# Kernel optimization log

Measured on AMD Instinct MI355X. Metric: run time of the kernel, lower is better.

Reference implementation:

```python
import jax, jax.numpy as jnp
import numpy as np

N = 50000      # nodes
E = 500000     # edges
D = 128        # in_dim == out_dim
L = 4          # encoder_layers
G = 64         # graphs in batch
FIXED = 10000  # fixed_input_dim
BN_EPS = 1e-5


def setup_inputs() -> dict:
    key = jax.random.key(0)
    ks = jax.random.split(key, 14)
    s = 0.05
    feat_id = jax.random.randint(ks[0], (N,), 0, FIXED)
    edge_index = jax.random.randint(ks[1], (2, E), 0, N)
    # sorted graph assignment guaranteeing all G graphs are non-empty
    batch = (jnp.arange(N) * G) // N
    return {
        "feat_id": feat_id,
        "edge_index": edge_index,
        "batch": batch,
        # value_projection: Linear(FIXED, D); store weight.T as a lookup table
        "value_proj_w": jax.random.normal(ks[2], (FIXED, D)) * s,
        "value_proj_b": jax.random.normal(ks[3], (D,)) * s,
        "deg_emb": jax.random.normal(ks[4], (1001, D)) * s,
        # stacked per-layer GIN MLP params: Linear -> BN -> ReLU -> Linear
        "mlp_w1": jax.random.normal(ks[5], (L, D, D)) * s,
        "mlp_b1": jax.random.normal(ks[6], (L, D)) * s,
        "bn1_g": 1.0 + 0.1 * jax.random.normal(ks[7], (L, D)),
        "bn1_b": 0.1 * jax.random.normal(ks[8], (L, D)),
        "mlp_w2": jax.random.normal(ks[9], (L, D, D)) * s,
        "mlp_b2": jax.random.normal(ks[10], (L, D)) * s,
        # outer per-layer BatchNorm1d
        "bn2_g": 1.0 + 0.1 * jax.random.normal(ks[11], (L, D)),
        "bn2_b": 0.1 * jax.random.normal(ks[12], (L, D)),
    }


def _bn(x, g, b):
    # BatchNorm1d in training mode: batch stats over the node axis, biased var
    mu = jnp.mean(x, axis=0)
    var = jnp.mean(jnp.square(x - mu), axis=0)
    return g * (x - mu) * jax.lax.rsqrt(var + BN_EPS) + b


def reference(feat_id, edge_index, batch, value_proj_w, value_proj_b, deg_emb,
              mlp_w1, mlp_b1, bn1_g, bn1_b, mlp_w2, mlp_b2, bn2_g, bn2_b):
    src, dst = edge_index[0], edge_index[1]
    # one_hot(feat_id % FIXED) @ W.T + b  ==  gather of transposed weight rows
    h_attr = value_proj_w[feat_id % FIXED] + value_proj_b  # [N, D]
    # in-degree embedding (clamped to [0, 1000])
    in_deg = jax.ops.segment_sum(jnp.ones((E,), jnp.int32), dst, num_segments=N)
    h = h_attr + deg_emb[jnp.clip(in_deg, 0, 1000)]
    for i in range(L):
        # GIN: sum_{j in N(v)} h_j + (1 + eps) * h_v, eps = 0 (learn_eps=False)
        agg = jax.ops.segment_sum(h[src], dst, num_segments=N) + h
        z = jax.nn.relu(_bn(agg @ mlp_w1[i] + mlp_b1[i], bn1_g[i], bn1_b[i]))
        z = z @ mlp_w2[i] + mlp_b2[i]
        h = jax.nn.relu(_bn(z, bn2_g[i], bn2_b[i]))
    # global mean pool per graph
    gsum = jax.ops.segment_sum(h, batch, num_segments=G)       # [G, D]
    cnt = jax.ops.segment_sum(jnp.ones((N, 1)), batch, num_segments=G)
    graph_feature = gsum / jnp.maximum(cnt, 1.0)
    return graph_feature, h
```

## Files before the change

kernel.cpp:

```cpp
#include <hip/hip_runtime.h>

#define NN 50000
#define NE 500000
#define DD 128
#define NL 4
#define NG 64
#define FIXED_DIM 10000
#define BN_EPS 1e-5f
#define NB 196

typedef unsigned short u16;
typedef unsigned int u32;
typedef __attribute__((ext_vector_type(8))) short bf16x8;
typedef __attribute__((ext_vector_type(4))) float f32x4;

__device__ __forceinline__ float bf2f(u16 u) {
    return __uint_as_float(((u32)u) << 16);
}
__device__ __forceinline__ u16 f2bf(float f) {
    u32 u = __float_as_uint(f);
    return (u16)((u + 0x7FFFu + ((u >> 16) & 1u)) >> 16);
}
__device__ __forceinline__ float ldf(const void* p, size_t i, int isbf) {
    return isbf ? bf2f(((const u16*)p)[i]) : ((const float*)p)[i];
}

__global__ void k_pre(const void* __restrict__ vb, int* __restrict__ flag,
                      const int* __restrict__ batch, int* __restrict__ goff,
                      float* __restrict__ zbase, int zwords) {
    int b = blockIdx.x, t = threadIdx.x;
    if (b == 0) {
        __shared__ int ok[256];
        float v = (t < 128) ? bf2f(((const u16*)vb)[t]) : 0.f;
        ok[t] = (t < 128) ? ((fabsf(v) < 1000.f) ? 1 : 0) : 1;
        __syncthreads();
        for (int off = 128; off; off >>= 1) {
            if (t < off) ok[t] &= ok[t + off];
            __syncthreads();
        }
        if (t == 0) *flag = ok[0];
    } else if (b == 1) {
        if (t <= NG) {
            int lo = 0, hi = NN;
            while (lo < hi) {
                int mid = (lo + hi) >> 1;
                if (batch[mid] < t) lo = mid + 1; else hi = mid;
            }
            goff[t] = lo;
        }
    } else {
        int i = (b - 2) * 256 + t;
        if (i < zwords) zbase[i] = 0.f;
    }
}

__global__ void k_cvt6(const void* b1, const void* b2, const void* g1,
                       const void* be1, const void* g2, const void* be2,
                       float* __restrict__ pc, const int* __restrict__ flag) {
    int t = blockIdx.x * 256 + threadIdx.x;
    if (t >= 6 * NL * DD) return;
    int p = t >> 9, j = t & 511;
    const void* s = (p == 0) ? b1 : (p == 1) ? b2 : (p == 2) ? g1
                  : (p == 3) ? be1 : (p == 4) ? g2 : be2;
    pc[t] = ldf(s, j, *flag);
}
__global__ void k_deg(const int* __restrict__ dst, int* __restrict__ deg) {
    int i = blockIdx.x * 256 + threadIdx.x;
    if (i < NE) atomicAdd(&deg[dst[i]], 1);
}

__global__ void k_scan1(const int* __restrict__ deg, int* __restrict__ bsum) {
    __shared__ int S[256];
    int b = blockIdx.x, t = threadIdx.x;
    int i = b * 256 + t;
    S[t] = (i < NN) ? deg[i] : 0;
    __syncthreads();
    for (int off = 128; off; off >>= 1) {
        if (t < off) S[t] += S[t + off];
        __syncthreads();
    }
    if (t == 0) bsum[b] = S[0];
}
__global__ void k_scan2(int* __restrict__ bsum) {
    __shared__ int S[256];
    int t = threadIdx.x;
    int v = (t < NB) ? bsum[t] : 0;
    S[t] = v;
    __syncthreads();
    for (int off = 1; off < 256; off <<= 1) {
        int x = (t >= off) ? S[t - off] : 0;
        __syncthreads();
        S[t] += x;
        __syncthreads();
    }
    if (t < NB) bsum[t] = S[t] - v;
}
__global__ void k_scan3(const int* __restrict__ deg, const int* __restrict__ bsum,
                        int* __restrict__ rowptr) {
    __shared__ int S[256];
    int b = blockIdx.x, t = threadIdx.x;
    int i = b * 256 + t;
    int v = (i < NN) ? deg[i] : 0;
    S[t] = v;
    __syncthreads();
    for (int off = 1; off < 256; off <<= 1) {
        int x = (t >= off) ? S[t - off] : 0;
        __syncthreads();
        S[t] += x;
        __syncthreads();
    }
    if (i < NN) rowptr[i] = bsum[b] + S[t] - v;
    if (i == NN - 1) rowptr[NN] = bsum[b] + S[t];
}

__global__ void k_fill(const int* __restrict__ src, const int* __restrict__ dst,
                       const int* __restrict__ rowptr, int* __restrict__ cursor,
                       int* __restrict__ colidx) {
    int e = blockIdx.x * 256 + threadIdx.x;
    if (e >= NE) return;
    int d = dst[e];
    int p = atomicAdd(&cursor[d], 1);
    colidx[rowptr[d] + p] = src[e];
}

__global__ void k_swz(const void* __restrict__ w1, const void* __restrict__ w2,
                      u16* __restrict__ Wsw, const int* __restrict__ flag) {
    int t = blockIdx.x * 256 + threadIdx.x;
    if (t >= 8 * 16384) return;
    int m    = t >> 14;
    int idx  = t & 16383;
    int nt   = idx >> 11;
    int ks   = (idx >> 9) & 3;
    int lane = (idx >> 3) & 63;
    int j    = idx & 7;
    int row = ks * 32 + (lane >> 4) * 8 + j;
    int col = nt * 16 + (lane & 15);
    const void* src = (m < 4) ? w1 : w2;
    size_t off = (size_t)(m & 3) * DD * DD + (size_t)row * DD + col;
    Wsw[t] = f2bf(ldf(src, off, *flag));
}

__global__ void k_init(const int* __restrict__ feat, const int* __restrict__ deg,
                       const void* __restrict__ vw, const void* __restrict__ vb,
                       const void* __restrict__ demb, u16* __restrict__ B,
                       const int* __restrict__ flag) {
    int t = blockIdx.x * 256 + threadIdx.x;
    if (t >= NN * DD) return;
    int n = t >> 7, c = t & 127;
    int isbf = *flag;
    int f = feat[n] % FIXED_DIM;
    int dg = min(deg[n], 1000);
    B[t] = f2bf(ldf(vw, (size_t)f * DD + c, isbf)
              + ldf(vb, c, isbf)
              + ldf(demb, (size_t)dg * DD + c, isbf));
}

template <bool AFF>
__global__ __launch_bounds__(256, 8) void k_aggr(
        const u16* __restrict__ B, const int* __restrict__ rowptr,
        const int* __restrict__ colidx,
        const float* __restrict__ gIn, const float* __restrict__ bIn,
        const float* __restrict__ sIn, const float* __restrict__ qIn,
        u16* __restrict__ Agg) {
    int n = blockIdx.x * 4 + (threadIdx.x >> 6);
    if (n >= NN) return;
    int c = (threadIdx.x & 63) * 2;
    float a0 = 1.f, b0 = 0.f, a1 = 1.f, b1 = 0.f;
    if (AFF) {
        float inv = 1.0f / (float)NN;
        float mu0 = sIn[c] * inv, mu1 = sIn[c + 1] * inv;
        float v0 = fmaxf(qIn[c] * inv - mu0 * mu0, 0.f);
        float v1 = fmaxf(qIn[c + 1] * inv - mu1 * mu1, 0.f);
        a0 = gIn[c] * rsqrtf(v0 + BN_EPS);
        a1 = gIn[c + 1] * rsqrtf(v1 + BN_EPS);
        b0 = bIn[c] - a0 * mu0;
        b1 = bIn[c + 1] - a1 * mu1;
    }
    u32 w = *(const u32*)&B[(size_t)n * DD + c];
    float x0 = bf2f((u16)(w & 0xFFFF)), x1 = bf2f((u16)(w >> 16));
    float s0 = AFF ? fmaxf(fmaf(a0, x0, b0), 0.f) : x0;
    float s1 = AFF ? fmaxf(fmaf(a1, x1, b1), 0.f) : x1;
    int lo = rowptr[n], hi = rowptr[n + 1];
    int j = lo;
    for (; j + 4 <= hi; j += 4) {
        int m0 = colidx[j], m1 = colidx[j + 1];
        int m2 = colidx[j + 2], m3 = colidx[j + 3];
        u32 w0 = *(const u32*)&B[(size_t)m0 * DD + c];
        u32 w1v = *(const u32*)&B[(size_t)m1 * DD + c];
        u32 w2v = *(const u32*)&B[(size_t)m2 * DD + c];
        u32 w3v = *(const u32*)&B[(size_t)m3 * DD + c];
        float y;
        y = bf2f((u16)(w0 & 0xFFFF)); s0 += AFF ? fmaxf(fmaf(a0, y, b0), 0.f) : y;
        y = bf2f((u16)(w0 >> 16));    s1 += AFF ? fmaxf(fmaf(a1, y, b1), 0.f) : y;
        y = bf2f((u16)(w1v & 0xFFFF)); s0 += AFF ? fmaxf(fmaf(a0, y, b0), 0.f) : y;
        y = bf2f((u16)(w1v >> 16));    s1 += AFF ? fmaxf(fmaf(a1, y, b1), 0.f) : y;
        y = bf2f((u16)(w2v & 0xFFFF)); s0 += AFF ? fmaxf(fmaf(a0, y, b0), 0.f) : y;
        y = bf2f((u16)(w2v >> 16));    s1 += AFF ? fmaxf(fmaf(a1, y, b1), 0.f) : y;
        y = bf2f((u16)(w3v & 0xFFFF)); s0 += AFF ? fmaxf(fmaf(a0, y, b0), 0.f) : y;
        y = bf2f((u16)(w3v >> 16));    s1 += AFF ? fmaxf(fmaf(a1, y, b1), 0.f) : y;
    }
    for (; j < hi; j++) {
        int m = colidx[j];
        w = *(const u32*)&B[(size_t)m * DD + c];
        x0 = bf2f((u16)(w & 0xFFFF)); x1 = bf2f((u16)(w >> 16));
        s0 += AFF ? fmaxf(fmaf(a0, x0, b0), 0.f) : x0;
        s1 += AFF ? fmaxf(fmaf(a1, x1, b1), 0.f) : x1;
    }
    *(u32*)&Agg[(size_t)n * DD + c] = ((u32)f2bf(s1) << 16) | (u32)f2bf(s0);
}

template <bool IN16, bool OUT16, bool AFF>
__global__ __launch_bounds__(256, 2) void k_gemm(
        const void* In, const u16* __restrict__ Wsw,
        const float* __restrict__ bias,
        const float* __restrict__ gIn, const float* __restrict__ bIn,
        const float* __restrict__ sIn, const float* __restrict__ qIn,
        void* Out, float* __restrict__ ssum, float* __restrict__ ssq,
        int nRows) {
    __shared__ u16 Wl[16384];
    __shared__ u16 At[128 * 136];
    __shared__ float affS[256];
    float* RedS = (float*)At;
    float* RedQ = RedS + 512;
    const int t = threadIdx.x;
    const int row0 = blockIdx.x * 128;

    if (AFF) {
        if (t < 128) {
            float inv = 1.0f / (float)NN;
            float mu = sIn[t] * inv;
            float var = fmaxf(qIn[t] * inv - mu * mu, 0.f);
            float a = gIn[t] * rsqrtf(var + BN_EPS);
            affS[t] = a;
            affS[128 + t] = bIn[t] - a * mu;
        }
        __syncthreads();
    }

    {
        const uint4* s = (const uint4*)Wsw;
        uint4* d = (uint4*)Wl;
        #pragma unroll
        for (int i = 0; i < 8; i++) d[t + i * 256] = s[t + i * 256];
    }
    if (IN16) {
        for (int i = t; i < 2048; i += 256) {
            int r  = i >> 4;
            int c8 = (i & 15) * 8;
            int gr = row0 + r;
            uint4 v = make_uint4(0u, 0u, 0u, 0u);
            if (gr < nRows) v = *(const uint4*)&((const u16*)In)[(size_t)gr * DD + c8];
            *(uint4*)&At[r * 136 + c8] = v;
        }
    } else {
        for (int i = t; i < 4096; i += 256) {
            int r  = i >> 5;
            int c4 = (i & 31) * 4;
            int gr = row0 + r;
            float4 v = make_float4(0.f, 0.f, 0.f, 0.f);
            if (gr < nRows) {
                v = *(const float4*)&((const float*)In)[(size_t)gr * DD + c4];
                if (AFF) {
                    v.x = fmaxf(fmaf(affS[c4 + 0], v.x, affS[128 + c4 + 0]), 0.f);
                    v.y = fmaxf(fmaf(affS[c4 + 1], v.y, affS[128 + c4 + 1]), 0.f);
                    v.z = fmaxf(fmaf(affS[c4 + 2], v.z, affS[128 + c4 + 2]), 0.f);
                    v.w = fmaxf(fmaf(affS[c4 + 3], v.w, affS[128 + c4 + 3]), 0.f);
                }
            }
            ushort4 o;
            o.x = f2bf(v.x); o.y = f2bf(v.y); o.z = f2bf(v.z); o.w = f2bf(v.w);
            *(ushort4*)&At[r * 136 + c4] = o;
        }
    }
    __syncthreads();

    const int w    = t >> 6;
    const int ln   = t & 63;
    const int quad = ln >> 4;
    const int lq   = ln & 15;

    f32x4 acc0[8], acc1[8];
    #pragma unroll
    for (int nt = 0; nt < 8; nt++) {
        acc0[nt] = (f32x4){0.f, 0.f, 0.f, 0.f};
        acc1[nt] = (f32x4){0.f, 0.f, 0.f, 0.f};
    }

    const u16* aRow0 = &At[(w * 32 + lq) * 136 + quad * 8];
    const u16* aRow1 = &At[(w * 32 + 16 + lq) * 136 + quad * 8];
    #pragma unroll
    for (int ks = 0; ks < 4; ks++) {
        bf16x8 a0 = *(const bf16x8*)&aRow0[ks * 32];
        bf16x8 a1 = *(const bf16x8*)&aRow1[ks * 32];
        #pragma unroll
        for (int nt = 0; nt < 8; nt++) {
            bf16x8 b = *(const bf16x8*)&Wl[((nt * 4 + ks) * 64 + ln) * 8];
            acc0[nt] = __builtin_amdgcn_mfma_f32_16x16x32_bf16(a0, b, acc0[nt], 0, 0, 0);
            acc1[nt] = __builtin_amdgcn_mfma_f32_16x16x32_bf16(a1, b, acc1[nt], 0, 0, 0);
        }
    }
    __syncthreads();

    const int rb0 = row0 + w * 32 + quad * 4;
    const int rb1 = rb0 + 16;
    #pragma unroll
    for (int nt = 0; nt < 8; nt++) {
        int col = nt * 16 + lq;
        float bv = bias[col];
        float s = 0.f, q = 0.f;
        #pragma unroll
        for (int r = 0; r < 4; r++) {
            int gr = rb0 + r;
            if (gr < nRows) {
                float val = acc0[nt][r] + bv;
                size_t o = (size_t)gr * DD + col;
                if (OUT16) ((u16*)Out)[o] = f2bf(val);
                else       ((float*)Out)[o] = val;
                s += val; q += val * val;
            }
        }
        #pragma unroll
        for (int r = 0; r < 4; r++) {
            int gr = rb1 + r;
            if (gr < nRows) {
                float val = acc1[nt][r] + bv;
                size_t o = (size_t)gr * DD + col;
                if (OUT16) ((u16*)Out)[o] = f2bf(val);
                else       ((float*)Out)[o] = val;
                s += val; q += val * val;
            }
        }
        s += __shfl_xor(s, 16); q += __shfl_xor(q, 16);
        s += __shfl_xor(s, 32); q += __shfl_xor(q, 32);
        if (quad == 0) { RedS[w * 128 + col] = s; RedQ[w * 128 + col] = q; }
    }
    __syncthreads();
    if (t < 128) {
        float s = RedS[t] + RedS[128 + t] + RedS[256 + t] + RedS[384 + t];
        float q = RedQ[t] + RedQ[128 + t] + RedQ[256 + t] + RedQ[384 + t];
        atomicAdd(&ssum[t], s);
        atomicAdd(&ssq[t], q);
    }
}

__global__ __launch_bounds__(256, 4) void k_update2(
        const u16* __restrict__ Bz,
        const float* __restrict__ gIn, const float* __restrict__ bIn,
        const float* __restrict__ sIn, const float* __restrict__ qIn,
        const int* __restrict__ batch, float* __restrict__ A,
        float* __restrict__ gsum) {
    const int t = threadIdx.x;
    const int c = t & 127;
    const int half = t >> 7;
    const int r0 = blockIdx.x * 64;
    float inv = 1.0f / (float)NN;
    float mu = sIn[c] * inv;
    float var = fmaxf(qIn[c] * inv - mu * mu, 0.f);
    float a = gIn[c] * rsqrtf(var + BN_EPS);
    float bb = bIn[c] - a * mu;
    float acc = 0.f;
    int curg = -1;
    for (int i = 0; i < 32; i++) {
        int r = r0 + half + 2 * i;
        if (r >= NN) break;
        int gg = batch[r];
        if (gg != curg) {
            if (curg >= 0) atomicAdd(&gsum[(size_t)curg * DD + c], acc);
            acc = 0.f; curg = gg;
        }
        float v = fmaxf(fmaf(a, bf2f(Bz[(size_t)r * DD + c]), bb), 0.f);
        A[(size_t)r * DD + c] = v;
        acc += v;
    }
    if (curg >= 0) atomicAdd(&gsum[(size_t)curg * DD + c], acc);
}

__global__ void k_pool2(const float* __restrict__ gsum, const int* __restrict__ goff,
                        float* __restrict__ out) {
    int t = blockIdx.x * 256 + threadIdx.x;
    int g = t >> 7;
    float cnt = fmaxf((float)(goff[g + 1] - goff[g]), 1.0f);
    out[t] = gsum[t] / cnt;
}

extern "C" void kernel_launch(void* const* d_in, const int* in_sizes, int n_in,
                              void* d_out, int out_size, void* d_ws, size_t ws_size,
                              hipStream_t stream) {
    const int* feat  = (const int*)d_in[0];
    const int* ei    = (const int*)d_in[1];
    const int* batch = (const int*)d_in[2];
    const void* vw   = d_in[3];
    const void* vb   = d_in[4];
    const void* demb = d_in[5];
    const void* w1   = d_in[6];
    const void* b1   = d_in[7];
    const void* g1   = d_in[8];
    const void* be1  = d_in[9];
    const void* w2   = d_in[10];
    const void* b2   = d_in[11];
    const void* g2   = d_in[12];
    const void* be2  = d_in[13];

    const int* src = ei;
    const int* dst = ei + NE;
    const size_t ND = (size_t)NN * DD;

    float* pc     = (float*)d_ws;
    int*   flag   = (int*)(pc + 3072);
    float* stats  = (float*)(flag + 64);
    float* gsum   = stats + 2048;
    int*   deg    = (int*)(gsum + 8192);
    int*   cursor = deg + NN;
    int*   bsum   = cursor + NN;
    int*   goff   = bsum + 256;
    int*   rowptr = goff + 128;
    int*   colidx = rowptr + NN + 64;
    u16*   Wsw    = (u16*)(colidx + NE);
    u16*   B      = Wsw + 8 * 16384;
    u16*   Agg16  = B + ND;

    float* b1c  = pc;
    float* b2c  = pc + 512;
    float* g1c  = pc + 1024;
    float* be1c = pc + 1536;
    float* g2c  = pc + 2048;
    float* be2c = pc + 2560;
    float* sum1 = stats;
    float* sq1  = stats + 512;
    float* sum2 = stats + 1024;
    float* sq2  = stats + 1536;

    float* outw = (float*)d_out;
    float* A    = outw + (size_t)NG * DD;

    const int zwords = 2048 + 8192 + NN + NN;
    const int gridND = (int)((ND + 255) / 256);
    const int gemmBlocks = (NN + 127) / 128;
    const int aggrBlocks = (NN + 3) / 4;

    k_pre<<<2 + (zwords + 255) / 256, 256, 0, stream>>>(vb, flag, batch, goff,
                                                        stats, zwords);
    k_cvt6<<<(6 * NL * DD + 255) / 256, 256, 0, stream>>>(b1, b2, g1, be1, g2, be2, pc, flag);
    k_swz<<<(8 * 16384) / 256, 256, 0, stream>>>(w1, w2, Wsw, flag);
    k_deg<<<(NE + 255) / 256, 256, 0, stream>>>(dst, deg);
    k_scan1<<<NB, 256, 0, stream>>>(deg, bsum);
    k_scan2<<<1, 256, 0, stream>>>(bsum);
    k_scan3<<<NB, 256, 0, stream>>>(deg, bsum, rowptr);
    k_fill<<<(NE + 255) / 256, 256, 0, stream>>>(src, dst, rowptr, cursor, colidx);
    k_init<<<gridND, 256, 0, stream>>>(feat, deg, vw, vb, demb, B, flag);

    for (int l = 0; l < NL; l++) {
        const u16* W1l = Wsw + (size_t)l * 16384;
        const u16* W2l = Wsw + (size_t)(4 + l) * 16384;
        if (l == 0) {
            k_aggr<false><<<aggrBlocks, 256, 0, stream>>>(
                B, rowptr, colidx, nullptr, nullptr, nullptr, nullptr, Agg16);
        } else {
            k_aggr<true><<<aggrBlocks, 256, 0, stream>>>(
                B, rowptr, colidx, g2c + (l - 1) * 128, be2c + (l - 1) * 128,
                sum2 + (l - 1) * 128, sq2 + (l - 1) * 128, Agg16);
        }
        k_gemm<true, false, false><<<gemmBlocks, 256, 0, stream>>>(
            Agg16, W1l, b1c + l * 128, nullptr, nullptr, nullptr, nullptr,
            A, sum1 + l * 128, sq1 + l * 128, NN);
        k_gemm<false, true, true><<<gemmBlocks, 256, 0, stream>>>(
            A, W2l, b2c + l * 128, g1c + l * 128, be1c + l * 128,
            sum1 + l * 128, sq1 + l * 128,
            B, sum2 + l * 128, sq2 + l * 128, NN);
    }
    k_update2<<<(NN + 63) / 64, 256, 0, stream>>>(
        B, g2c + 3 * 128, be2c + 3 * 128, sum2 + 3 * 128, sq2 + 3 * 128,
        batch, A, gsum);
    k_pool2<<<(NG * DD + 255) / 256, 256, 0, stream>>>(gsum, goff, outw);
}
```

Measured before the change: 527.7 us.

## Fuse neighbor aggregation into first GEMM and merge setup kernels

Neighbor aggregation is fused with the first MLP linear layer. Each 64-row block gathers neighbor sums into shared memory as bf16, then multiplies by the weight tile with MFMA and accumulates BN statistics, so the intermediate aggregate never round-trips through global memory. Several small setup kernels are merged: the param conversion with the weight swizzle, scan1 with scan2 via a last-block semaphore, scan3 with init, and the final update with pooling. This cuts launch count. In exchange the fused kernel uses much more LDS and has lower occupancy (launch bounds 3), which may hurt latency hiding for the irregular gathers.

```diff
diff --git a/kernel.cpp b/kernel.cpp
--- a/kernel.cpp
+++ b/kernel.cpp
@@ -54,23 +54,43 @@
     }
 }
 
-__global__ void k_cvt6(const void* b1, const void* b2, const void* g1,
-                       const void* be1, const void* g2, const void* be2,
-                       float* __restrict__ pc, const int* __restrict__ flag) {
-    int t = blockIdx.x * 256 + threadIdx.x;
-    if (t >= 6 * NL * DD) return;
-    int p = t >> 9, j = t & 511;
-    const void* s = (p == 0) ? b1 : (p == 1) ? b2 : (p == 2) ? g1
-                  : (p == 3) ? be1 : (p == 4) ? g2 : be2;
-    pc[t] = ldf(s, j, *flag);
-}
+__global__ void k_cvtswz(const void* b1, const void* b2, const void* g1,
+                         const void* be1, const void* g2, const void* be2,
+                         const void* __restrict__ w1, const void* __restrict__ w2,
+                         float* __restrict__ pc, u16* __restrict__ Wsw,
+                         const int* __restrict__ flag) {
+    int b = blockIdx.x, tt = threadIdx.x;
+    if (b < 12) {
+        int t = b * 256 + tt;
+        int p = t >> 9, j = t & 511;
+        const void* s = (p == 0) ? b1 : (p == 1) ? b2 : (p == 2) ? g1
+                      : (p == 3) ? be1 : (p == 4) ? g2 : be2;
+        pc[t] = ldf(s, j, *flag);
+    } else {
+        int t = (b - 12) * 256 + tt;
+        int m    = t >> 14;
+        int idx  = t & 16383;
+        int nt   = idx >> 11;
+        int ks   = (idx >> 9) & 3;
+        int lane = (idx >> 3) & 63;
+        int j    = idx & 7;
+        int row = ks * 32 + (lane >> 4) * 8 + j;
+        int col = nt * 16 + (lane & 15);
+        const void* src = (m < 4) ? w1 : w2;
+        size_t off = (size_t)(m & 3) * DD * DD + (size_t)row * DD + col;
+        Wsw[t] = f2bf(ldf(src, off, *flag));
+    }
+}
+
 __global__ void k_deg(const int* __restrict__ dst, int* __restrict__ deg) {
     int i = blockIdx.x * 256 + threadIdx.x;
     if (i < NE) atomicAdd(&deg[dst[i]], 1);
 }
 
-__global__ void k_scan1(const int* __restrict__ deg, int* __restrict__ bsum) {
+__global__ void k_scan12(const int* __restrict__ deg, int* __restrict__ bsum,
+                         int* __restrict__ sem) {
     __shared__ int S[256];
+    __shared__ int lastB;
     int b = blockIdx.x, t = threadIdx.x;
     int i = b * 256 + t;
     S[t] = (i < NN) ? deg[i] : 0;
@@ -79,12 +99,15 @@
         if (t < off) S[t] += S[t + off];
         __syncthreads();
     }
-    if (t == 0) bsum[b] = S[0];
-}
-__global__ void k_scan2(int* __restrict__ bsum) {
-    __shared__ int S[256];
-    int t = threadIdx.x;
-    int v = (t < NB) ? bsum[t] : 0;
+    if (t == 0) {
+        atomicExch(&bsum[b], S[0]);
+        __threadfence();
+        lastB = (atomicAdd(&sem[0], 1) == gridDim.x - 1);
+    }
+    __syncthreads();
+    if (!lastB) return;
+    __threadfence();
+    int v = (t < NB) ? atomicAdd(&bsum[t], 0) : 0;
     S[t] = v;
     __syncthreads();
     for (int off = 1; off < 256; off <<= 1) {
@@ -95,22 +118,38 @@
     }
     if (t < NB) bsum[t] = S[t] - v;
 }
-__global__ void k_scan3(const int* __restrict__ deg, const int* __restrict__ bsum,
-                        int* __restrict__ rowptr) {
+
+__global__ void k_scan3init(const int* __restrict__ deg, const int* __restrict__ bsum,
+                            int* __restrict__ rowptr,
+                            const int* __restrict__ feat, const void* __restrict__ vw,
+                            const void* __restrict__ vb, const void* __restrict__ demb,
+                            u16* __restrict__ B, const int* __restrict__ flag) {
     __shared__ int S[256];
     int b = blockIdx.x, t = threadIdx.x;
-    int i = b * 256 + t;
-    int v = (i < NN) ? deg[i] : 0;
-    S[t] = v;
-    __syncthreads();
-    for (int off = 1; off < 256; off <<= 1) {
-        int x = (t >= off) ? S[t - off] : 0;
+    if (b < NB) {
+        int i = b * 256 + t;
+        int v = (i < NN) ? deg[i] : 0;
+        S[t] = v;
         __syncthreads();
-        S[t] += x;
-        __syncthreads();
-    }
-    if (i < NN) rowptr[i] = bsum[b] + S[t] - v;
-    if (i == NN - 1) rowptr[NN] = bsum[b] + S[t];
+        for (int off = 1; off < 256; off <<= 1) {
+            int x = (t >= off) ? S[t - off] : 0;
+            __syncthreads();
+            S[t] += x;
+            __syncthreads();
+        }
+        if (i < NN) rowptr[i] = bsum[b] + S[t] - v;
+        if (i == NN - 1) rowptr[NN] = bsum[b] + S[t];
+    } else {
+        int idx = (b - NB) * 256 + t;
+        if (idx >= NN * DD) return;
+        int n = idx >> 7, c = idx & 127;
+        int isbf = *flag;
+        int f = feat[n] % FIXED_DIM;
+        int dg = min(deg[n], 1000);
+        B[idx] = f2bf(ldf(vw, (size_t)f * DD + c, isbf)
+                    + ldf(vb, c, isbf)
+                    + ldf(demb, (size_t)dg * DD + c, isbf));
+    }
 }
 
 __global__ void k_fill(const int* __restrict__ src, const int* __restrict__ dst,
@@ -123,90 +162,129 @@
     colidx[rowptr[d] + p] = src[e];
 }
 
-__global__ void k_swz(const void* __restrict__ w1, const void* __restrict__ w2,
-                      u16* __restrict__ Wsw, const int* __restrict__ flag) {
-    int t = blockIdx.x * 256 + threadIdx.x;
-    if (t >= 8 * 16384) return;
-    int m    = t >> 14;
-    int idx  = t & 16383;
-    int nt   = idx >> 11;
-    int ks   = (idx >> 9) & 3;
-    int lane = (idx >> 3) & 63;
-    int j    = idx & 7;
-    int row = ks * 32 + (lane >> 4) * 8 + j;
-    int col = nt * 16 + (lane & 15);
-    const void* src = (m < 4) ? w1 : w2;
-    size_t off = (size_t)(m & 3) * DD * DD + (size_t)row * DD + col;
-    Wsw[t] = f2bf(ldf(src, off, *flag));
-}
-
-__global__ void k_init(const int* __restrict__ feat, const int* __restrict__ deg,
-                       const void* __restrict__ vw, const void* __restrict__ vb,
-                       const void* __restrict__ demb, u16* __restrict__ B,
-                       const int* __restrict__ flag) {
-    int t = blockIdx.x * 256 + threadIdx.x;
-    if (t >= NN * DD) return;
-    int n = t >> 7, c = t & 127;
-    int isbf = *flag;
-    int f = feat[n] % FIXED_DIM;
-    int dg = min(deg[n], 1000);
-    B[t] = f2bf(ldf(vw, (size_t)f * DD + c, isbf)
-              + ldf(vb, c, isbf)
-              + ldf(demb, (size_t)dg * DD + c, isbf));
-}
-
 template <bool AFF>
-__global__ __launch_bounds__(256, 8) void k_aggr(
-        const u16* __restrict__ B, const int* __restrict__ rowptr,
-        const int* __restrict__ colidx,
+__global__ __launch_bounds__(256, 3) void k_ag1(
+        const u16* __restrict__ Bv, const int* __restrict__ rowptr,
+        const int* __restrict__ colidx, const u16* __restrict__ Wsw,
+        const float* __restrict__ bias,
         const float* __restrict__ gIn, const float* __restrict__ bIn,
         const float* __restrict__ sIn, const float* __restrict__ qIn,
-        u16* __restrict__ Agg) {
-    int n = blockIdx.x * 4 + (threadIdx.x >> 6);
-    if (n >= NN) return;
-    int c = (threadIdx.x & 63) * 2;
-    float a0 = 1.f, b0 = 0.f, a1 = 1.f, b1 = 0.f;
-    if (AFF) {
-        float inv = 1.0f / (float)NN;
-        float mu0 = sIn[c] * inv, mu1 = sIn[c + 1] * inv;
-        float v0 = fmaxf(qIn[c] * inv - mu0 * mu0, 0.f);
-        float v1 = fmaxf(qIn[c + 1] * inv - mu1 * mu1, 0.f);
-        a0 = gIn[c] * rsqrtf(v0 + BN_EPS);
-        a1 = gIn[c + 1] * rsqrtf(v1 + BN_EPS);
-        b0 = bIn[c] - a0 * mu0;
-        b1 = bIn[c + 1] - a1 * mu1;
-    }
-    u32 w = *(const u32*)&B[(size_t)n * DD + c];
-    float x0 = bf2f((u16)(w & 0xFFFF)), x1 = bf2f((u16)(w >> 16));
-    float s0 = AFF ? fmaxf(fmaf(a0, x0, b0), 0.f) : x0;
-    float s1 = AFF ? fmaxf(fmaf(a1, x1, b1), 0.f) : x1;
-    int lo = rowptr[n], hi = rowptr[n + 1];
-    int j = lo;
-    for (; j + 4 <= hi; j += 4) {
-        int m0 = colidx[j], m1 = colidx[j + 1];
-        int m2 = colidx[j + 2], m3 = colidx[j + 3];
-        u32 w0 = *(const u32*)&B[(size_t)m0 * DD + c];
-        u32 w1v = *(const u32*)&B[(size_t)m1 * DD + c];
-        u32 w2v = *(const u32*)&B[(size_t)m2 * DD + c];
-        u32 w3v = *(const u32*)&B[(size_t)m3 * DD + c];
-        float y;
-        y = bf2f((u16)(w0 & 0xFFFF)); s0 += AFF ? fmaxf(fmaf(a0, y, b0), 0.f) : y;
-        y = bf2f((u16)(w0 >> 16));    s1 += AFF ? fmaxf(fmaf(a1, y, b1), 0.f) : y;
-        y = bf2f((u16)(w1v & 0xFFFF)); s0 += AFF ? fmaxf(fmaf(a0, y, b0), 0.f) : y;
-        y = bf2f((u16)(w1v >> 16));    s1 += AFF ? fmaxf(fmaf(a1, y, b1), 0.f) : y;
-        y = bf2f((u16)(w2v & 0xFFFF)); s0 += AFF ? fmaxf(fmaf(a0, y, b0), 0.f) : y;
-        y = bf2f((u16)(w2v >> 16));    s1 += AFF ? fmaxf(fmaf(a1, y, b1), 0.f) : y;
-        y = bf2f((u16)(w3v & 0xFFFF)); s0 += AFF ? fmaxf(fmaf(a0, y, b0), 0.f) : y;
-        y = bf2f((u16)(w3v >> 16));    s1 += AFF ? fmaxf(fmaf(a1, y, b1), 0.f) : y;
-    }
-    for (; j < hi; j++) {
-        int m = colidx[j];
-        w = *(const u32*)&B[(size_t)m * DD + c];
-        x0 = bf2f((u16)(w & 0xFFFF)); x1 = bf2f((u16)(w >> 16));
-        s0 += AFF ? fmaxf(fmaf(a0, x0, b0), 0.f) : x0;
-        s1 += AFF ? fmaxf(fmaf(a1, x1, b1), 0.f) : x1;
-    }
-    *(u32*)&Agg[(size_t)n * DD + c] = ((u32)f2bf(s1) << 16) | (u32)f2bf(s0);
+        float* __restrict__ Out, float* __restrict__ ssum, float* __restrict__ ssq) {
+    __shared__ u16 Wl[16384];
+    __shared__ u16 At[64 * 136];
+    float* RedS = (float*)At;
+    float* RedQ = RedS + 512;
+    const int t = threadIdx.x;
+    const int w = t >> 6;
+    const int ln = t & 63;
+    const int row0 = blockIdx.x * 64;
+
+    {
+        const uint4* s = (const uint4*)Wsw;
+        uint4* d = (uint4*)Wl;
+        #pragma unroll
+        for (int i = 0; i < 8; i++) d[t + i * 256] = s[t + i * 256];
+    }
+
+    {
+        const int c = ln * 2;
+        float a0 = 1.f, b0 = 0.f, a1 = 1.f, b1 = 0.f;
+        if (AFF) {
+            float inv = 1.0f / (float)NN;
+            float mu0 = sIn[c] * inv, mu1 = sIn[c + 1] * inv;
+            float v0 = fmaxf(qIn[c] * inv - mu0 * mu0, 0.f);
+            float v1 = fmaxf(qIn[c + 1] * inv - mu1 * mu1, 0.f);
+            a0 = gIn[c] * rsqrtf(v0 + BN_EPS);
+            a1 = gIn[c + 1] * rsqrtf(v1 + BN_EPS);
+            b0 = bIn[c] - a0 * mu0;
+            b1 = bIn[c + 1] - a1 * mu1;
+        }
+        for (int rr = 0; rr < 16; rr++) {
+            int lr = w * 16 + rr;
+            int gr = row0 + lr;
+            float s0 = 0.f, s1 = 0.f;
+            if (gr < NN) {
+                u32 wd = *(const u32*)&Bv[(size_t)gr * DD + c];
+                float x0 = bf2f((u16)(wd & 0xFFFF)), x1 = bf2f((u16)(wd >> 16));
+                s0 = AFF ? fmaxf(fmaf(a0, x0, b0), 0.f) : x0;
+                s1 = AFF ? fmaxf(fmaf(a1, x1, b1), 0.f) : x1;
+                int lo = rowptr[gr], hi = rowptr[gr + 1];
+                int j = lo;
+                for (; j + 4 <= hi; j += 4) {
+                    int m0 = colidx[j], m1 = colidx[j + 1];
+                    int m2 = colidx[j + 2], m3 = colidx[j + 3];
+                    u32 wd0 = *(const u32*)&Bv[(size_t)m0 * DD + c];
+                    u32 wd1 = *(const u32*)&Bv[(size_t)m1 * DD + c];
+                    u32 wd2 = *(const u32*)&Bv[(size_t)m2 * DD + c];
+                    u32 wd3 = *(const u32*)&Bv[(size_t)m3 * DD + c];
+                    float y;
+                    y = bf2f((u16)(wd0 & 0xFFFF)); s0 += AFF ? fmaxf(fmaf(a0, y, b0), 0.f) : y;
+                    y = bf2f((u16)(wd0 >> 16));    s1 += AFF ? fmaxf(fmaf(a1, y, b1), 0.f) : y;
+                    y = bf2f((u16)(wd1 & 0xFFFF)); s0 += AFF ? fmaxf(fmaf(a0, y, b0), 0.f) : y;
+                    y = bf2f((u16)(wd1 >> 16));    s1 += AFF ? fmaxf(fmaf(a1, y, b1), 0.f) : y;
+                    y = bf2f((u16)(wd2 & 0xFFFF)); s0 += AFF ? fmaxf(fmaf(a0, y, b0), 0.f) : y;
+                    y = bf2f((u16)(wd2 >> 16));    s1 += AFF ? fmaxf(fmaf(a1, y, b1), 0.f) : y;
+                    y = bf2f((u16)(wd3 & 0xFFFF)); s0 += AFF ? fmaxf(fmaf(a0, y, b0), 0.f) : y;
+                    y = bf2f((u16)(wd3 >> 16));    s1 += AFF ? fmaxf(fmaf(a1, y, b1), 0.f) : y;
+                }
+                for (; j < hi; j++) {
+                    int m = colidx[j];
+                    u32 wd2 = *(const u32*)&Bv[(size_t)m * DD + c];
+                    float y0 = bf2f((u16)(wd2 & 0xFFFF)), y1 = bf2f((u16)(wd2 >> 16));
+                    s0 += AFF ? fmaxf(fmaf(a0, y0, b0), 0.f) : y0;
+                    s1 += AFF ? fmaxf(fmaf(a1, y1, b1), 0.f) : y1;
+                }
+            }
+            *(u32*)&At[lr * 136 + c] = ((u32)f2bf(s1) << 16) | (u32)f2bf(s0);
+        }
+    }
+    __syncthreads();
+
+    const int quad = ln >> 4;
+    const int lq   = ln & 15;
+
+    f32x4 acc[8];
+    #pragma unroll
+    for (int nt = 0; nt < 8; nt++) acc[nt] = (f32x4){0.f, 0.f, 0.f, 0.f};
+
+    const u16* aRow = &At[(w * 16 + lq) * 136 + quad * 8];
+    #pragma unroll
+    for (int ks = 0; ks < 4; ks++) {
+        bf16x8 a = *(const bf16x8*)&aRow[ks * 32];
+        #pragma unroll
+        for (int nt = 0; nt < 8; nt++) {
+            bf16x8 b = *(const bf16x8*)&Wl[((nt * 4 + ks) * 64 + ln) * 8];
+            acc[nt] = __builtin_amdgcn_mfma_f32_16x16x32_bf16(a, b, acc[nt], 0, 0, 0);
+        }
+    }
+    __syncthreads();
+
+    const int rb = row0 + w * 16 + quad * 4;
+    #pragma unroll
+    for (int nt = 0; nt < 8; nt++) {
+        int col = nt * 16 + lq;
+        float bv = bias[col];
+        float s = 0.f, q = 0.f;
+        #pragma unroll
+        for (int r = 0; r < 4; r++) {
+            int gr = rb + r;
+            if (gr < NN) {
+                float val = acc[nt][r] + bv;
+                Out[(size_t)gr * DD + col] = val;
+                s += val; q += val * val;
+            }
+        }
+        s += __shfl_xor(s, 16); q += __shfl_xor(q, 16);
+        s += __shfl_xor(s, 32); q += __shfl_xor(q, 32);
+        if (quad == 0) { RedS[w * 128 + col] = s; RedQ[w * 128 + col] = q; }
+    }
+    __syncthreads();
+    if (t < 128) {
+        float s = RedS[t] + RedS[128 + t] + RedS[256 + t] + RedS[384 + t];
+        float q = RedQ[t] + RedQ[128 + t] + RedQ[256 + t] + RedQ[384 + t];
+        atomicAdd(&ssum[t], s);
+        atomicAdd(&ssq[t], q);
+    }
 }
 
 template <bool IN16, bool OUT16, bool AFF>
@@ -343,12 +421,13 @@
     }
 }
 
-__global__ __launch_bounds__(256, 4) void k_update2(
+__global__ __launch_bounds__(256, 4) void k_upool(
         const u16* __restrict__ Bz,
         const float* __restrict__ gIn, const float* __restrict__ bIn,
         const float* __restrict__ sIn, const float* __restrict__ qIn,
         const int* __restrict__ batch, float* __restrict__ A,
-        float* __restrict__ gsum) {
+        float* __restrict__ gsum, const int* __restrict__ goff,
+        float* __restrict__ outw, int* __restrict__ sem) {
     const int t = threadIdx.x;
     const int c = t & 127;
     const int half = t >> 7;
@@ -373,14 +452,20 @@
         acc += v;
     }
     if (curg >= 0) atomicAdd(&gsum[(size_t)curg * DD + c], acc);
-}
-
-__global__ void k_pool2(const float* __restrict__ gsum, const int* __restrict__ goff,
-                        float* __restrict__ out) {
-    int t = blockIdx.x * 256 + threadIdx.x;
-    int g = t >> 7;
-    float cnt = fmaxf((float)(goff[g + 1] - goff[g]), 1.0f);
-    out[t] = gsum[t] / cnt;
+
+    __shared__ int lastF;
+    if (t == 0) {
+        __threadfence();
+        lastF = (atomicAdd(&sem[1], 1) == gridDim.x - 1);
+    }
+    __syncthreads();
+    if (!lastF) return;
+    __threadfence();
+    for (int i = t; i < NG * DD; i += 256) {
+        int g = i >> 7;
+        float cnt = fmaxf((float)(goff[g + 1] - goff[g]), 1.0f);
+        outw[i] = atomicAdd(&gsum[i], 0.0f) / cnt;
+    }
 }
 
 extern "C" void kernel_launch(void* const* d_in, const int* in_sizes, int n_in,
@@ -411,13 +496,13 @@
     float* gsum   = stats + 2048;
     int*   deg    = (int*)(gsum + 8192);
     int*   cursor = deg + NN;
-    int*   bsum   = cursor + NN;
+    int*   sem    = cursor + NN;
+    int*   bsum   = sem + 64;
     int*   goff   = bsum + 256;
     int*   rowptr = goff + 128;
     int*   colidx = rowptr + NN + 64;
     u16*   Wsw    = (u16*)(colidx + NE);
     u16*   B      = Wsw + 8 * 16384;
-    u16*   Agg16  = B + ND;
 
     float* b1c  = pc;
     float* b2c  = pc + 512;
@@ -433,43 +518,42 @@
     float* outw = (float*)d_out;
     float* A    = outw + (size_t)NG * DD;
 
-    const int zwords = 2048 + 8192 + NN + NN;
-    const int gridND = (int)((ND + 255) / 256);
+    const int zwords = 2048 + 8192 + NN + NN + 64;
+    const int gridND = (int)(ND / 256);
     const int gemmBlocks = (NN + 127) / 128;
-    const int aggrBlocks = (NN + 3) / 4;
+    const int agBlocks   = (NN + 63) / 64;
 
     k_pre<<<2 + (zwords + 255) / 256, 256, 0, stream>>>(vb, flag, batch, goff,
                                                         stats, zwords);
-    k_cvt6<<<(6 * NL * DD + 255) / 256, 256, 0, stream>>>(b1, b2, g1, be1, g2, be2, pc, flag);
-    k_swz<<<(8 * 16384) / 256, 256, 0, stream>>>(w1, w2, Wsw, flag);
+    k_cvtswz<<<12 + 512, 256, 0, stream>>>(b1, b2, g1, be1, g2, be2, w1, w2,
+                                           pc, Wsw, flag);
     k_deg<<<(NE + 255) / 256, 256, 0, stream>>>(dst, deg);
-    k_scan1<<<NB, 256, 0, stream>>>(deg, bsum);
-    k_scan2<<<1, 256, 0, stream>>>(bsum);
-    k_scan3<<<NB, 256, 0, stream>>>(deg, bsum, rowptr);
+    k_scan12<<<NB, 256, 0, stream>>>(deg, bsum, sem);
+    k_scan3init<<<NB + gridND, 256, 0, stream>>>(deg, bsum, rowptr,
+                                                 feat, vw, vb, demb, B, flag);
     k_fill<<<(NE + 255) / 256, 256, 0, stream>>>(src, dst, rowptr, cursor, colidx);
-    k_init<<<gridND, 256, 0, stream>>>(feat, deg, vw, vb, demb, B, flag);
 
     for (int l = 0; l < NL; l++) {
         const u16* W1l = Wsw + (size_t)l * 16384;
         const u16* W2l = Wsw + (size_t)(4 + l) * 16384;
         if (l == 0) {
-            k_aggr<false><<<aggrBlocks, 256, 0, stream>>>(
-                B, rowptr, colidx, nullptr, nullptr, nullptr, nullptr, Agg16);
+            k_ag1<false><<<agBlocks, 256, 0, stream>>>(
+                B, rowptr, colidx, W1l, b1c + l * 128,
+                nullptr, nullptr, nullptr, nullptr,
+                A, sum1 + l * 128, sq1 + l * 128);
         } else {
-            k_aggr<true><<<aggrBlocks, 256, 0, stream>>>(
-                B, rowptr, colidx, g2c + (l - 1) * 128, be2c + (l - 1) * 128,
-                sum2 + (l - 1) * 128, sq2 + (l - 1) * 128, Agg16);
-        }
-        k_gemm<true, false, false><<<gemmBlocks, 256, 0, stream>>>(
-            Agg16, W1l, b1c + l * 128, nullptr, nullptr, nullptr, nullptr,
-            A, sum1 + l * 128, sq1 + l * 128, NN);
+            k_ag1<true><<<agBlocks, 256, 0, stream>>>(
+                B, rowptr, colidx, W1l, b1c + l * 128,
+                g2c + (l - 1) * 128, be2c + (l - 1) * 128,
+                sum2 + (l - 1) * 128, sq2 + (l - 1) * 128,
+                A, sum1 + l * 128, sq1 + l * 128);
+        }
         k_gemm<false, true, true><<<gemmBlocks, 256, 0, stream>>>(
             A, W2l, b2c + l * 128, g1c + l * 128, be1c + l * 128,
             sum1 + l * 128, sq1 + l * 128,
             B, sum2 + l * 128, sq2 + l * 128, NN);
     }
-    k_update2<<<(NN + 63) / 64, 256, 0, stream>>>(
+    k_upool<<<(NN + 63) / 64, 256, 0, stream>>>(
         B, g2c + 3 * 128, be2c + 3 * 128, sum2 + 3 * 128, sq2 + 3 * 128,
-        batch, A, gsum);
-    k_pool2<<<(NG * DD + 255) / 256, 256, 0, stream>>>(gsum, goff, outw);
-}
+        batch, A, gsum, goff, outw, sem);
+}
```

Result: slower. 776.3 us (+47.1%).
